# Kernel tuning notes

Hardware: AMD Instinct MI355X
Metric: run time of the kernel (lower is better)

The kernel has to match this reference:

```python
import jax, jax.numpy as jnp
import numpy as np

# Model dims
B, T, D = 2, 2048, 768
H, DH = 12, 64          # attention heads, head_dim = D // H
IH, ID = 4, 64          # indexer heads, indexer dim
K = 64                  # top_k selected KV tokens per query


def setup_inputs() -> dict:
    key = jax.random.key(0)
    ks = jax.random.split(key, 10)
    s = 0.02
    return {
        "x": jax.random.normal(ks[0], (B, T, D), jnp.float32),
        # lightning indexer projections (nn.Linear weights are [out, in])
        "wq_i": jax.random.normal(ks[1], (IH * ID, D), jnp.float32) * s,
        "bq_i": jnp.zeros((IH * ID,), jnp.float32),
        "wk_i": jax.random.normal(ks[2], (IH * ID, D), jnp.float32) * s,
        "bk_i": jnp.zeros((IH * ID,), jnp.float32),
        "w_head": jax.random.normal(ks[3], (IH,), jnp.float32),
        # fused qkv + out projections
        "w_qkv": jax.random.normal(ks[4], (3 * D, D), jnp.float32) * s,
        "b_qkv": jnp.zeros((3 * D,), jnp.float32),
        "w_out": jax.random.normal(ks[5], (D, D), jnp.float32) * s,
        "b_out": jnp.zeros((D,), jnp.float32),
    }


def reference(x, wq_i, bq_i, wk_i, bk_i, w_head, w_qkv, b_qkv, w_out, b_out):
    Bb, Tt, Dd = x.shape
    # fused QKV: [B,T,3,H,DH]
    qkv = (x @ w_qkv.T + b_qkv).reshape(Bb, Tt, 3, H, DH)
    q, k, v = qkv[:, :, 0], qkv[:, :, 1], qkv[:, :, 2]  # each [B,T,H,DH]

    # lightning indexer: I[b,t,s] = sum_h w_h * relu(qI[b,t,h] . kI[b,s,h])
    qI = (x @ wq_i.T + bq_i).reshape(Bb, Tt, IH, ID)
    kI = (x @ wk_i.T + bk_i).reshape(Bb, Tt, IH, ID)
    rel = jax.nn.relu(jnp.einsum('bthd,bshd->bhts', qI, kI))  # [B,IH,T,T]
    scores = jnp.einsum('h,bhts->bts', w_head, rel)           # [B,T,T]

    # causal mask, then top-k KV selection per query
    causal = jnp.tril(jnp.ones((Tt, Tt), dtype=bool))
    scores = jnp.where(causal[None], scores, -jnp.inf)
    vals, idx = jax.lax.top_k(scores, K)                      # [B,T,K]
    valid = jnp.isfinite(vals)                                # early queries have < K causal keys
    routing = jnp.where(valid, vals, 0.0)                     # routing weights = scores * valid

    # gather selected K/V tokens (shared across attention heads)
    gather = jax.vmap(lambda arr, i: arr[i])                  # per-batch fancy gather
    k_sel = gather(k, idx)                                    # [B,T,K,H,DH]
    v_sel = gather(v, idx)                                    # [B,T,K,H,DH]

    # sparse attention over the K selected tokens
    att = jnp.einsum('bthd,btkhd->bhtk', q, k_sel) / jnp.sqrt(jnp.float32(DH))
    att = jnp.where(valid[:, None], att, -jnp.inf)            # mask invalid slots
    p = jax.nn.softmax(att, axis=-1)                          # [B,H,T,K]
    p = p * routing[:, None]                                  # indexer routing gate
    out = jnp.einsum('bhtk,btkhd->bthd', p, v_sel).reshape(Bb, Tt, Dd)
    return out @ w_out.T + b_out
```

## Files before the change

kernel.cpp:

```cpp
#include <hip/hip_runtime.h>
#include <hip/hip_bf16.h>
#include <math.h>

#define B_   2
#define T_   2048
#define D_   768
#define H_   12
#define DH_  64
#define IH_  4
#define ID_  64
#define K_   64
#define M_   (B_ * T_)
#define NQKV 2304

#define LDT 132

typedef __attribute__((ext_vector_type(8))) short bf16x8;
typedef __attribute__((ext_vector_type(4))) float f32x4;

#define GLOBAL_AS __attribute__((address_space(1)))
#define LDS_AS    __attribute__((address_space(3)))

__device__ __forceinline__ void split2(float f, unsigned short& h, unsigned short& l)
{
    __bf16 b = (__bf16)f;
    h = __builtin_bit_cast(unsigned short, b);
    __bf16 c = (__bf16)(f - (float)b);
    l = __builtin_bit_cast(unsigned short, c);
}

__global__ __launch_bounds__(256) void split_kernel(
    const float* __restrict__ in, unsigned short* __restrict__ hi,
    unsigned short* __restrict__ lo, int n4)
{
    int i = blockIdx.x * 256 + threadIdx.x;
    if (i >= n4) return;
    float4 v = ((const float4*)in)[i];
    ushort4 hv, lv;
    split2(v.x, hv.x, lv.x);
    split2(v.y, hv.y, lv.y);
    split2(v.z, hv.z, lv.z);
    split2(v.w, hv.w, lv.w);
    ((ushort4*)hi)[i] = hv;
    ((ushort4*)lo)[i] = lv;
}

__global__ __launch_bounds__(256) void gemm_bf16split(
    const unsigned short* __restrict__ Ahi, const unsigned short* __restrict__ Alo,
    const unsigned short* __restrict__ Whi, const unsigned short* __restrict__ Wlo,
    const float* __restrict__ bias, float* __restrict__ C, int Nn)
{
    __shared__ char lsa[128 * 128];
    __shared__ char lsb[128 * 128];
    const int tid = threadIdx.x;
    const int lane = tid & 63;
    const int wv = tid >> 6;
    const int bm = blockIdx.y * 128, bn = blockIdx.x * 128;
    const int wr = (wv >> 1) * 64, wc = (wv & 1) * 64;

    f32x4 acc[4][4];
    const f32x4 zero = {0.0f, 0.0f, 0.0f, 0.0f};
#pragma unroll
    for (int m = 0; m < 4; ++m)
#pragma unroll
        for (int n = 0; n < 4; ++n) acc[m][n] = zero;

    const int srow = lane >> 3;
    const int scol = (lane & 7) * 16;

    for (int kt = 0; kt < 36; ++kt) {
        const unsigned short* Ap;
        const unsigned short* Wp;
        int kc;
        if (kt < 12)      { Ap = Ahi; Wp = Whi; kc = kt * 64; }
        else if (kt < 24) { Ap = Ahi; Wp = Wlo; kc = (kt - 12) * 64; }
        else              { Ap = Alo; Wp = Whi; kc = (kt - 24) * 64; }

#pragma unroll
        for (int i = 0; i < 4; ++i) {
            int rl = wv * 32 + i * 8 + srow;
            int sb = scol ^ ((rl & 7) << 4);
            const char* ga = (const char*)Ap + ((size_t)(bm + rl) * D_ + kc) * 2 + sb;
            __builtin_amdgcn_global_load_lds((GLOBAL_AS const void*)ga,
                (LDS_AS void*)(lsa + (wv * 32 + i * 8) * 128), 16, 0, 0);
            const char* gb = (const char*)Wp + ((size_t)(bn + rl) * D_ + kc) * 2 + sb;
            __builtin_amdgcn_global_load_lds((GLOBAL_AS const void*)gb,
                (LDS_AS void*)(lsb + (wv * 32 + i * 8) * 128), 16, 0, 0);
        }
        __syncthreads();

#pragma unroll
        for (int ks = 0; ks < 2; ++ks) {
            bf16x8 afr[4], bfr[4];
            const int kb = ks * 64 + ((lane >> 4) * 16);
#pragma unroll
            for (int m = 0; m < 4; ++m) {
                int r = wr + m * 16 + (lane & 15);
                afr[m] = *(const bf16x8*)(lsa + r * 128 + (kb ^ ((r & 7) << 4)));
                int rn = wc + m * 16 + (lane & 15);
                bfr[m] = *(const bf16x8*)(lsb + rn * 128 + (kb ^ ((rn & 7) << 4)));
            }
#pragma unroll
            for (int m = 0; m < 4; ++m)
#pragma unroll
                for (int n = 0; n < 4; ++n)
                    acc[m][n] = __builtin_amdgcn_mfma_f32_16x16x32_bf16(
                        afr[m], bfr[n], acc[m][n], 0, 0, 0);
        }
        __syncthreads();
    }

    float bv[4];
#pragma unroll
    for (int n = 0; n < 4; ++n) bv[n] = bias[bn + wc + n * 16 + (lane & 15)];
#pragma unroll
    for (int m = 0; m < 4; ++m)
#pragma unroll
        for (int n = 0; n < 4; ++n)
#pragma unroll
            for (int j = 0; j < 4; ++j) {
                int row = bm + wr + m * 16 + (lane >> 4) * 4 + j;
                int col = bn + wc + n * 16 + (lane & 15);
                C[(size_t)row * Nn + col] = acc[m][n][j] + bv[n];
            }
}

__global__ __launch_bounds__(256) void gemm_qiki64(
    const float* __restrict__ x,
    const float* __restrict__ wq, const float* __restrict__ bq,
    const float* __restrict__ wk, const float* __restrict__ bk,
    float* __restrict__ qI, float* __restrict__ kI)
{
    __shared__ float la[32][LDT];
    __shared__ float lb[32][68];
    const int tid = threadIdx.x;
    const int tx = tid & 15, ty = tid >> 4;
    const int bm = blockIdx.y * 128;
    int bn = blockIdx.x * 64;
    const float* W; const float* bias; float* Out;
    if (bn < 256) { W = wq; bias = bq; Out = qI; }
    else          { W = wk; bias = bk; Out = kI; bn -= 256; }

    float acc[8][4];
#pragma unroll
    for (int i = 0; i < 8; ++i)
#pragma unroll
        for (int j = 0; j < 4; ++j) acc[i][j] = 0.0f;

    for (int k0 = 0; k0 < D_; k0 += 32) {
#pragma unroll
        for (int i = 0; i < 4; ++i) {
            int f4 = tid + (i << 8);
            int r = f4 >> 3, cq = f4 & 7;
            float4 a = *(const float4*)(x + (size_t)(bm + r) * D_ + k0 + (cq << 2));
            la[cq * 4 + 0][r] = a.x;
            la[cq * 4 + 1][r] = a.y;
            la[cq * 4 + 2][r] = a.z;
            la[cq * 4 + 3][r] = a.w;
        }
#pragma unroll
        for (int i = 0; i < 2; ++i) {
            int f4 = tid + (i << 8);
            int r = f4 >> 3, cq = f4 & 7;
            float4 w4 = *(const float4*)(W + (size_t)(bn + r) * D_ + k0 + (cq << 2));
            lb[cq * 4 + 0][r] = w4.x;
            lb[cq * 4 + 1][r] = w4.y;
            lb[cq * 4 + 2][r] = w4.z;
            lb[cq * 4 + 3][r] = w4.w;
        }
        __syncthreads();
#pragma unroll
        for (int kk = 0; kk < 32; ++kk) {
            float4 a0 = *(const float4*)&la[kk][ty * 8];
            float4 a1 = *(const float4*)&la[kk][ty * 8 + 4];
            float4 b0 = *(const float4*)&lb[kk][tx * 4];
            float av[8] = {a0.x, a0.y, a0.z, a0.w, a1.x, a1.y, a1.z, a1.w};
            float bv4[4] = {b0.x, b0.y, b0.z, b0.w};
#pragma unroll
            for (int i = 0; i < 8; ++i)
#pragma unroll
                for (int j = 0; j < 4; ++j)
                    acc[i][j] = fmaf(av[i], bv4[j], acc[i][j]);
        }
        __syncthreads();
    }

    float bs[4];
    {
        float4 q0 = *(const float4*)(bias + bn + tx * 4);
        bs[0] = q0.x; bs[1] = q0.y; bs[2] = q0.z; bs[3] = q0.w;
    }
#pragma unroll
    for (int i = 0; i < 8; ++i) {
        int rr = bm + ty * 8 + i;
        float4 o;
        o.x = acc[i][0] + bs[0];
        o.y = acc[i][1] + bs[1];
        o.z = acc[i][2] + bs[2];
        o.w = acc[i][3] + bs[3];
        *(float4*)(Out + (size_t)rr * (IH_ * ID_) + bn + tx * 4) = o;
    }
}

__global__ __launch_bounds__(256) void scores_kernel(
    const float* __restrict__ qI, const float* __restrict__ kI,
    const float* __restrict__ w_head, float* __restrict__ scores)
{
    const int is = blockIdx.x, it = blockIdx.y, b = blockIdx.z;
    if (is > it) return;
    __shared__ float lq[32][LDT];
    __shared__ float lk[32][LDT];
    const int tid = threadIdx.x;
    const int tx = tid & 15, ty = tid >> 4;
    const int t0 = it * 128, s0 = is * 128;

    float sc[8][8];
#pragma unroll
    for (int i = 0; i < 8; ++i)
#pragma unroll
        for (int j = 0; j < 8; ++j) sc[i][j] = 0.0f;

    for (int h = 0; h < IH_; ++h) {
        float rel[8][8];
#pragma unroll
        for (int i = 0; i < 8; ++i)
#pragma unroll
            for (int j = 0; j < 8; ++j) rel[i][j] = 0.0f;

        for (int k0 = 0; k0 < ID_; k0 += 32) {
#pragma unroll
            for (int i = 0; i < 4; ++i) {
                int f4 = tid + (i << 8);
                int r = f4 >> 3;
                int cq = f4 & 7;
                float4 a = *(const float4*)(qI + (size_t)(b * T_ + t0 + r) * (IH_ * ID_) + h * ID_ + k0 + (cq << 2));
                lq[cq * 4 + 0][r] = a.x;
                lq[cq * 4 + 1][r] = a.y;
                lq[cq * 4 + 2][r] = a.z;
                lq[cq * 4 + 3][r] = a.w;
                float4 c = *(const float4*)(kI + (size_t)(b * T_ + s0 + r) * (IH_ * ID_) + h * ID_ + k0 + (cq << 2));
                lk[cq * 4 + 0][r] = c.x;
                lk[cq * 4 + 1][r] = c.y;
                lk[cq * 4 + 2][r] = c.z;
                lk[cq * 4 + 3][r] = c.w;
            }
            __syncthreads();
#pragma unroll
            for (int kk = 0; kk < 32; ++kk) {
                float4 a0 = *(const float4*)&lq[kk][ty * 8];
                float4 a1 = *(const float4*)&lq[kk][ty * 8 + 4];
                float4 b0 = *(const float4*)&lk[kk][tx * 8];
                float4 b1 = *(const float4*)&lk[kk][tx * 8 + 4];
                float av[8] = {a0.x, a0.y, a0.z, a0.w, a1.x, a1.y, a1.z, a1.w};
                float bv[8] = {b0.x, b0.y, b0.z, b0.w, b1.x, b1.y, b1.z, b1.w};
#pragma unroll
                for (int i = 0; i < 8; ++i)
#pragma unroll
                    for (int j = 0; j < 8; ++j)
                        rel[i][j] = fmaf(av[i], bv[j], rel[i][j]);
            }
            __syncthreads();
        }
        float wh = w_head[h];
#pragma unroll
        for (int i = 0; i < 8; ++i)
#pragma unroll
            for (int j = 0; j < 8; ++j)
                sc[i][j] += wh * fmaxf(rel[i][j], 0.0f);
    }

#pragma unroll
    for (int i = 0; i < 8; ++i) {
        int tt = t0 + ty * 8 + i;
        float* sp = scores + ((size_t)b * T_ + tt) * T_ + s0 + tx * 8;
        float4 o0 = {sc[i][0], sc[i][1], sc[i][2], sc[i][3]};
        float4 o1 = {sc[i][4], sc[i][5], sc[i][6], sc[i][7]};
        *(float4*)sp = o0;
        *(float4*)(sp + 4) = o1;
    }
}

__global__ __launch_bounds__(256) void topk_kernel(
    const float* __restrict__ scores, int* __restrict__ idx_out,
    float* __restrict__ rout_out)
{
    const int row = blockIdx.x;
    const int b = row >> 11;
    const int t = row & (T_ - 1);
    const int tid = threadIdx.x;
    const int lane = tid & 63;
    const int wv = tid >> 6;
    const int n = t + 1;
    const float* srow = scores + ((size_t)b * T_ + t) * T_;
    const size_t obase = (size_t)row * K_;

    if (n <= K_) {
        for (int r = tid; r < K_; r += 256) {
            idx_out[obase + r] = (r < n) ? r : 0;
            rout_out[obase + r] = (r < n) ? srow[r] : 0.0f;
        }
        return;
    }

    __shared__ unsigned int keys[T_];
    __shared__ unsigned int hist[256];
    __shared__ unsigned int nb[256];
    __shared__ int wt0[4], wt1[4];
    __shared__ unsigned int sh_prefix;
    __shared__ int sh_need;

    for (int s = tid; s < n; s += 256) {
        unsigned int u = __float_as_uint(srow[s]);
        u ^= (u & 0x80000000u) ? 0xffffffffu : 0x80000000u;
        keys[s] = u;
    }

    unsigned int prefix = 0;
    int need = K_;
    for (int pass = 0; pass < 4; ++pass) {
        const int shift = 24 - pass * 8;
        const unsigned int pmask = (pass == 0) ? 0u : (0xffffffffu << (shift + 8));
        hist[tid] = 0;
        __syncthreads();
        for (int s = tid; s < n; s += 256) {
            unsigned int k = keys[s];
            if ((k & pmask) == prefix)
                atomicAdd(&hist[(k >> shift) & 0xffu], 1u);
        }
        __syncthreads();
        int v = (int)hist[tid];
#pragma unroll
        for (int off = 1; off < 64; off <<= 1) {
            int o = __shfl_down(v, off);
            if (lane + off < 64) v += o;
        }
        if (lane == 0) wt0[wv] = v;
        __syncthreads();
        int wadd = 0;
#pragma unroll
        for (int w2 = 0; w2 < 4; ++w2) if (w2 > wv) wadd += wt0[w2];
        int sfx = v + wadd;
        nb[tid] = (unsigned)sfx;
        __syncthreads();
        int sfx1 = (tid < 255) ? (int)nb[tid + 1] : 0;
        if (sfx >= need && sfx1 < need) {
            sh_prefix = prefix | ((unsigned)tid << shift);
            sh_need = need - sfx1;
        }
        __syncthreads();
        prefix = sh_prefix;
        need = sh_need;
        __syncthreads();
    }
    const unsigned int thr = prefix;

    const int chunk = (n + 255) >> 8;
    const int base = tid * chunk;
    int cg = 0, ce = 0;
    for (int j = 0; j < chunk; ++j) {
        int s = base + j;
        if (s < n) {
            unsigned int k = keys[s];
            cg += (k > thr);
            ce += (k == thr);
        }
    }
    int vg = cg, ve = ce;
#pragma unroll
    for (int off = 1; off < 64; off <<= 1) {
        int og = __shfl_up(vg, off);
        int oe = __shfl_up(ve, off);
        if (lane >= off) { vg += og; ve += oe; }
    }
    if (lane == 63) { wt0[wv] = vg; wt1[wv] = ve; }
    __syncthreads();
    int offg = 0, offe = 0, G = 0;
#pragma unroll
    for (int w2 = 0; w2 < 4; ++w2) {
        G += wt0[w2];
        if (w2 < wv) { offg += wt0[w2]; offe += wt1[w2]; }
    }
    int sg = vg + offg - cg;
    int se = ve + offe - ce;
    for (int j = 0; j < chunk; ++j) {
        int s = base + j;
        if (s < n) {
            unsigned int k = keys[s];
            if (k >= thr) {
                unsigned int u = k ^ ((k & 0x80000000u) ? 0x80000000u : 0xffffffffu);
                if (k > thr) {
                    idx_out[obase + sg] = s;
                    rout_out[obase + sg] = __uint_as_float(u);
                    sg++;
                } else {
                    if (se < need) {
                        idx_out[obase + G + se] = s;
                        rout_out[obase + G + se] = __uint_as_float(u);
                    }
                    se++;
                }
            }
        }
    }
}

__global__ __launch_bounds__(256) void attn_kernel(
    const float* __restrict__ qkv, const int* __restrict__ idx,
    const float* __restrict__ routing,
    unsigned short* __restrict__ atthi, unsigned short* __restrict__ attlo)
{
    const int row = blockIdx.x;
    const int b = row >> 11;
    const int t = row & (T_ - 1);
    const int tid = threadIdx.x;
    const int lane = tid & 63;
    const int wave = tid >> 6;
    const int nv = (t + 1) < K_ ? (t + 1) : K_;

    __shared__ float qs[D_];
    for (int i = tid; i < D_; i += 256) qs[i] = qkv[(size_t)row * NQKV + i];

    int myidx = 0;
    float myrout = 0.0f;
    if (lane < nv) {
        myidx = idx[(size_t)row * K_ + lane];
        myrout = routing[(size_t)row * K_ + lane];
    }
    __syncthreads();

    const float scale = 0.125f;
#pragma unroll
    for (int hh = 0; hh < 3; ++hh) {
        const int h = wave + hh * 4;
        float att = -INFINITY;
        if (lane < nv) {
            const float* kp = qkv + (size_t)(b * T_ + myidx) * NQKV + D_ + h * DH_;
            const float* qp = qs + h * DH_;
            float acc = 0.0f;
#pragma unroll
            for (int d4 = 0; d4 < 16; ++d4) {
                float4 kv4 = *(const float4*)(kp + d4 * 4);
                float4 q4 = *(const float4*)(qp + d4 * 4);
                acc = fmaf(kv4.x, q4.x, acc);
                acc = fmaf(kv4.y, q4.y, acc);
                acc = fmaf(kv4.z, q4.z, acc);
                acc = fmaf(kv4.w, q4.w, acc);
            }
            att = acc * scale;
        }
        float m = att;
#pragma unroll
        for (int off = 32; off; off >>= 1) m = fmaxf(m, __shfl_xor(m, off));
        float e = (lane < nv) ? __expf(att - m) : 0.0f;
        float ssum = e;
#pragma unroll
        for (int off = 32; off; off >>= 1) ssum += __shfl_xor(ssum, off);
        float p = e / ssum * myrout;

        float acc = 0.0f;
        for (int k = 0; k < nv; ++k) {
            float pk = __shfl(p, k);
            int ik = __shfl(myidx, k);
            acc = fmaf(pk, qkv[(size_t)(b * T_ + ik) * NQKV + 2 * D_ + h * DH_ + lane], acc);
        }
        unsigned short h16, l16;
        split2(acc, h16, l16);
        atthi[(size_t)row * D_ + h * DH_ + lane] = h16;
        attlo[(size_t)row * D_ + h * DH_ + lane] = l16;
    }
}

extern "C" void kernel_launch(void* const* d_in, const int* in_sizes, int n_in,
                              void* d_out, int out_size, void* d_ws, size_t ws_size,
                              hipStream_t stream)
{
    const float* x      = (const float*)d_in[0];
    const float* wq_i   = (const float*)d_in[1];
    const float* bq_i   = (const float*)d_in[2];
    const float* wk_i   = (const float*)d_in[3];
    const float* bk_i   = (const float*)d_in[4];
    const float* w_head = (const float*)d_in[5];
    const float* w_qkv  = (const float*)d_in[6];
    const float* b_qkv  = (const float*)d_in[7];
    const float* w_out  = (const float*)d_in[8];
    const float* b_out  = (const float*)d_in[9];
    float* out = (float*)d_out;

    char* w = (char*)d_ws;
    float* scoresb        = (float*)w;
    unsigned short* wqh   = (unsigned short*)w;
    unsigned short* wql   = (unsigned short*)(w + 4194304);
    unsigned short* woh   = (unsigned short*)(w + 8388608);
    unsigned short* wol   = (unsigned short*)(w + 12582912);
    float* qkv            = (float*)(w + 33554432);
    float* qI             = (float*)(w + 71303168);
    float* kI             = (float*)(w + 75497472);
    float* routing        = (float*)(w + 79691776);
    int*   idxb           = (int*)  (w + 80740352);
    unsigned short* xhi   = (unsigned short*)(w + 81788928);
    unsigned short* xlo   = (unsigned short*)(w + 88080384);
    unsigned short* atthi = xhi;
    unsigned short* attlo = xlo;

    dim3 blk(256);

    split_kernel<<<dim3((M_ * D_ / 4 + 255) / 256), blk, 0, stream>>>(x, xhi, xlo, M_ * D_ / 4);
    split_kernel<<<dim3((NQKV * D_ / 4 + 255) / 256), blk, 0, stream>>>(w_qkv, wqh, wql, NQKV * D_ / 4);

    gemm_bf16split<<<dim3(NQKV / 128, M_ / 128), blk, 0, stream>>>(xhi, xlo, wqh, wql, b_qkv, qkv, NQKV);

    gemm_qiki64<<<dim3(8, M_ / 128), blk, 0, stream>>>(x, wq_i, bq_i, wk_i, bk_i, qI, kI);

    scores_kernel<<<dim3(T_ / 128, T_ / 128, B_), blk, 0, stream>>>(qI, kI, w_head, scoresb);
    topk_kernel<<<dim3(M_), blk, 0, stream>>>(scoresb, idxb, routing);

    split_kernel<<<dim3((D_ * D_ / 4 + 255) / 256), blk, 0, stream>>>(w_out, woh, wol, D_ * D_ / 4);

    attn_kernel<<<dim3(M_), blk, 0, stream>>>(qkv, idxb, routing, atthi, attlo);

    gemm_bf16split<<<dim3(D_ / 128, M_ / 128), blk, 0, stream>>>(atthi, attlo, woh, wol, b_out, out, D_);
}
```

Before: 531.6 us.

## Vectorize sparse attention PV gather and swizzle row-to-block mapping

The P·V stage no longer loops serially over the selected keys with one scalar load per lane. Each wave now splits the keys across four 16-lane groups, loads float4 slices of V for three heads at once, and combines the partial sums with xor shuffles. Softmax weights and gathered row offsets go through shared memory, which adds an extra block barrier. The block index is also remapped so that adjacent blocks work on rows spaced apart, which may change L2 locality for the gathered K/V rows.

```diff
diff --git a/kernel.cpp b/kernel.cpp
--- a/kernel.cpp
+++ b/kernel.cpp
@@ -409,7 +409,8 @@
     const float* __restrict__ routing,
     unsigned short* __restrict__ atthi, unsigned short* __restrict__ attlo)
 {
-    const int row = blockIdx.x;
+    const int bid = blockIdx.x;
+    const int row = ((bid & 7) << 9) | (bid >> 3);
     const int b = row >> 11;
     const int t = row & (T_ - 1);
     const int tid = threadIdx.x;
@@ -418,6 +419,9 @@
     const int nv = (t + 1) < K_ ? (t + 1) : K_;
 
     __shared__ float qs[D_];
+    __shared__ int vboff[K_];
+    __shared__ float pbuf[4][3][K_];
+
     for (int i = tid; i < D_; i += 256) qs[i] = qkv[(size_t)row * NQKV + i];
 
     int myidx = 0;
@@ -426,6 +430,7 @@
         myidx = idx[(size_t)row * K_ + lane];
         myrout = routing[(size_t)row * K_ + lane];
     }
+    if (wave == 0) vboff[lane] = (b * T_ + myidx) * NQKV;
     __syncthreads();
 
     const float scale = 0.125f;
@@ -455,18 +460,80 @@
         float ssum = e;
 #pragma unroll
         for (int off = 32; off; off >>= 1) ssum += __shfl_xor(ssum, off);
-        float p = e / ssum * myrout;
-
-        float acc = 0.0f;
-        for (int k = 0; k < nv; ++k) {
-            float pk = __shfl(p, k);
-            int ik = __shfl(myidx, k);
-            acc = fmaf(pk, qkv[(size_t)(b * T_ + ik) * NQKV + 2 * D_ + h * DH_ + lane], acc);
-        }
-        unsigned short h16, l16;
-        split2(acc, h16, l16);
-        atthi[(size_t)row * D_ + h * DH_ + lane] = h16;
-        attlo[(size_t)row * D_ + h * DH_ + lane] = l16;
+        pbuf[wave][hh][lane] = e / ssum * myrout;
+    }
+    __syncthreads();
+
+    const int sub = lane >> 4;
+    const int dl = lane & 15;
+    float4 a0 = {0, 0, 0, 0}, a1 = {0, 0, 0, 0}, a2 = {0, 0, 0, 0};
+    const float* vbase = qkv + 2 * D_ + wave * DH_ + dl * 4;
+
+    if (nv == K_) {
+#pragma unroll
+        for (int j = 0; j < 16; ++j) {
+            const int k = sub * 16 + j;
+            float p0 = pbuf[wave][0][k];
+            float p1 = pbuf[wave][1][k];
+            float p2 = pbuf[wave][2][k];
+            const float* vp = vbase + vboff[k];
+            float4 v0 = *(const float4*)(vp);
+            float4 v1 = *(const float4*)(vp + 4 * DH_);
+            float4 v2 = *(const float4*)(vp + 8 * DH_);
+            a0.x = fmaf(p0, v0.x, a0.x); a0.y = fmaf(p0, v0.y, a0.y);
+            a0.z = fmaf(p0, v0.z, a0.z); a0.w = fmaf(p0, v0.w, a0.w);
+            a1.x = fmaf(p1, v1.x, a1.x); a1.y = fmaf(p1, v1.y, a1.y);
+            a1.z = fmaf(p1, v1.z, a1.z); a1.w = fmaf(p1, v1.w, a1.w);
+            a2.x = fmaf(p2, v2.x, a2.x); a2.y = fmaf(p2, v2.y, a2.y);
+            a2.z = fmaf(p2, v2.z, a2.z); a2.w = fmaf(p2, v2.w, a2.w);
+        }
+    } else {
+        int kc = nv - sub * 16;
+        kc = kc < 0 ? 0 : (kc > 16 ? 16 : kc);
+        for (int j = 0; j < kc; ++j) {
+            const int k = sub * 16 + j;
+            float p0 = pbuf[wave][0][k];
+            float p1 = pbuf[wave][1][k];
+            float p2 = pbuf[wave][2][k];
+            const float* vp = vbase + vboff[k];
+            float4 v0 = *(const float4*)(vp);
+            float4 v1 = *(const float4*)(vp + 4 * DH_);
+            float4 v2 = *(const float4*)(vp + 8 * DH_);
+            a0.x = fmaf(p0, v0.x, a0.x); a0.y = fmaf(p0, v0.y, a0.y);
+            a0.z = fmaf(p0, v0.z, a0.z); a0.w = fmaf(p0, v0.w, a0.w);
+            a1.x = fmaf(p1, v1.x, a1.x); a1.y = fmaf(p1, v1.y, a1.y);
+            a1.z = fmaf(p1, v1.z, a1.z); a1.w = fmaf(p1, v1.w, a1.w);
+            a2.x = fmaf(p2, v2.x, a2.x); a2.y = fmaf(p2, v2.y, a2.y);
+            a2.z = fmaf(p2, v2.z, a2.z); a2.w = fmaf(p2, v2.w, a2.w);
+        }
+    }
+
+#pragma unroll
+    for (int off = 16; off <= 32; off <<= 1) {
+        a0.x += __shfl_xor(a0.x, off); a0.y += __shfl_xor(a0.y, off);
+        a0.z += __shfl_xor(a0.z, off); a0.w += __shfl_xor(a0.w, off);
+        a1.x += __shfl_xor(a1.x, off); a1.y += __shfl_xor(a1.y, off);
+        a1.z += __shfl_xor(a1.z, off); a1.w += __shfl_xor(a1.w, off);
+        a2.x += __shfl_xor(a2.x, off); a2.y += __shfl_xor(a2.y, off);
+        a2.z += __shfl_xor(a2.z, off); a2.w += __shfl_xor(a2.w, off);
+    }
+
+    if (sub == 0) {
+        const float accs[3][4] = {{a0.x, a0.y, a0.z, a0.w},
+                                  {a1.x, a1.y, a1.z, a1.w},
+                                  {a2.x, a2.y, a2.z, a2.w}};
+#pragma unroll
+        for (int hh = 0; hh < 3; ++hh) {
+            const int h = wave + hh * 4;
+            ushort4 hv, lv;
+            split2(accs[hh][0], hv.x, lv.x);
+            split2(accs[hh][1], hv.y, lv.y);
+            split2(accs[hh][2], hv.z, lv.z);
+            split2(accs[hh][3], hv.w, lv.w);
+            const size_t o = ((size_t)row * D_ + h * DH_ + dl * 4) >> 2;
+            ((ushort4*)atthi)[o] = hv;
+            ((ushort4*)attlo)[o] = lv;
+        }
     }
 }
 
```

Result: faster. 486.9 us (-8.4%).
